# Kernel optimization log

Hardware: AMD Instinct MI355X
Metric: run time of the kernel (lower is better)

The kernel has to match this reference:

```python
import jax, jax.numpy as jnp
import numpy as np


def setup_inputs() -> dict:
    key = jax.random.key(0)
    k1, k2 = jax.random.split(key)
    B, T, H, D = 2, 2048, 16, 64          # batch, seq, heads, head_dim
    NUM_HASHES, NUM_BUCKETS = 4, 64
    hidden_states = jax.random.normal(k1, (B, T, H * D), dtype=jnp.float32)
    # equivalent of torch.randn rotations with fixed hash_seed
    random_rotations = jax.random.normal(k2, (H, D, NUM_HASHES, NUM_BUCKETS // 2), dtype=jnp.float32)
    return {"hidden_states": hidden_states, "random_rotations": random_rotations}


def reference(hidden_states, random_rotations):
    # hidden_states: [B, T, H*D]; random_rotations: [H, D, num_hashes, num_buckets//2]
    H, D, num_hashes, half = random_rotations.shape
    B, T, _ = hidden_states.shape
    # _split_hidden_size_dim: [B,T,H*D] -> [B,H,T,D]
    v = hidden_states.reshape(B, T, H, D).transpose(0, 2, 1, 3)
    # rotated: [B, H, num_hashes, T, num_buckets//2]
    rotated = jnp.einsum('bhtd,hdnr->bhntr', v, random_rotations)
    rotated = jnp.concatenate([rotated, -rotated], axis=-1)  # [..., num_buckets]
    buckets = jnp.argmax(rotated, axis=-1)                   # [B, H, num_hashes, T]
    b = buckets.transpose(0, 1, 3, 2)                        # [B, H, T, num_hashes]
    # m[b,h,i,j] = any_n (bucket_n(i) == bucket_n(j)); OR-accumulate over the
    # small fixed num_hashes axis to avoid a [B,H,T,T,num_hashes] intermediate.
    m = jnp.zeros((B, H, T, T), dtype=bool)
    for n in range(num_hashes):
        bn = b[..., n]
        m = m | (bn[:, :, :, None] == bn[:, :, None, :])
    return m
```

## Files before the change

### kernel.cpp

```cpp
#include <hip/hip_runtime.h>
#include <stdint.h>

#define BB 2
#define HH 16
#define TT 2048
#define DD 64
#define NHASH 4
#define NHALF 32

__global__ __launch_bounds__(256, 3) void lsh_buckets_kernel(
    const float* __restrict__ hs,
    const float* __restrict__ rot,
    uint32_t* __restrict__ words)
{
    __shared__ uint32_t lds[12288];
    float4* v4 = (float4*)lds;
    float4* r4 = (float4*)(lds + 4096);

    const int blk  = blockIdx.x;
    const int bh   = blk >> 5;
    const int tblk = blk & 31;
    const int b    = bh >> 4;
    const int h    = bh & 15;
    const int t0   = tblk * 64;
    const int tid  = threadIdx.x;
    const int n    = tid >> 6;
    const int lane = tid & 63;
    const int tg   = lane >> 3;
    const int rg   = lane & 7;

    #pragma unroll
    for (int p = 0; p < 4; ++p) {
        const int k  = tid + p * 256;
        const int t  = k >> 4;
        const int d4 = k & 15;
        const float4 f = ((const float4*)(hs + ((size_t)(b * TT + t0 + t)) * (HH * DD) + h * DD))[d4];
        v4[t * 16 + (d4 ^ (t >> 3))] = f;
    }
    {
        const float* rh = rot + (size_t)h * (DD * NHASH * NHALF);
        float* rf = (float*)r4;
        #pragma unroll
        for (int p = 0; p < 32; ++p) {
            const int g  = tid + p * 256;
            const int d  = g >> 7;
            const int nr = g & 127;
            const int nn = nr >> 5;
            const int r  = nr & 31;
            const int slot = (d >> 2) ^ (r >> 2);
            rf[((nn * 32 + r) * 16 + slot) * 4 + (d & 3)] = rh[g];
        }
    }
    __syncthreads();

    double acc[8][4];
    #pragma unroll
    for (int i = 0; i < 8; ++i)
        #pragma unroll
        for (int j = 0; j < 4; ++j) acc[i][j] = 0.0;

    const int vbase = tg * 8 * 16;
    const int rbase = (n * 32 + rg * 4) * 16;

    for (int s = 0; s < 16; ++s) {
        double rd[4][4];
        #pragma unroll
        for (int j = 0; j < 4; ++j) {
            const float4 rf = r4[rbase + j * 16 + (s ^ rg)];
            rd[j][0] = (double)rf.x; rd[j][1] = (double)rf.y;
            rd[j][2] = (double)rf.z; rd[j][3] = (double)rf.w;
        }
        #pragma unroll
        for (int i = 0; i < 8; ++i) {
            const float4 vf = v4[vbase + i * 16 + (s ^ tg)];
            const double v0 = (double)vf.x, v1 = (double)vf.y;
            const double v2 = (double)vf.z, v3 = (double)vf.w;
            #pragma unroll
            for (int j = 0; j < 4; ++j) {
                acc[i][j] += v0 * rd[j][0];
                acc[i][j] += v1 * rd[j][1];
                acc[i][j] += v2 * rd[j][2];
                acc[i][j] += v3 * rd[j][3];
            }
        }
    }

    __syncthreads();
    float*    vmaxL = (float*)lds;
    float*    vminL = (float*)(lds + 2304);
    uint32_t* imaxL = lds + 4608;
    uint32_t* iminL = lds + 6912;
    uint32_t* bkt   = lds + 9216;

    #pragma unroll
    for (int i = 0; i < 8; ++i) {
        const int t = tg * 8 + i;
        float fmx = -INFINITY; int imx = 0;
        float fmn =  INFINITY; int imn = 0;
        #pragma unroll
        for (int j = 0; j < 4; ++j) {
            const float f = (float)acc[i][j];
            const int   r = rg * 4 + j;
            if (f > fmx) { fmx = f; imx = r; }
            if (f < fmn) { fmn = f; imn = r; }
        }
        const int o = (n * 64 + t) * 9 + rg;
        vmaxL[o] = fmx; vminL[o] = fmn;
        imaxL[o] = (uint32_t)imx; iminL[o] = (uint32_t)imn;
    }
    __syncthreads();
    {
        const int nn = tid >> 6;
        const int t  = tid & 63;
        float fmx = -INFINITY; int imx = 0;
        float fmn =  INFINITY; int imn = 0;
        #pragma unroll
        for (int g = 0; g < 8; ++g) {
            const int o = (nn * 64 + t) * 9 + g;
            const float fx = vmaxL[o];
            const float fn = vminL[o];
            if (fx > fmx) { fmx = fx; imx = (int)imaxL[o]; }
            if (fn < fmn) { fmn = fn; imn = (int)iminL[o]; }
        }
        const uint32_t bucket = (fmx >= -fmn) ? (uint32_t)imx : (uint32_t)(NHALF + imn);
        bkt[nn * 64 + t] = bucket;
    }
    __syncthreads();
    if (tid < 64) {
        words[(size_t)bh * TT + t0 + tid] = bkt[tid]
                                          | (bkt[64  + tid] << 8)
                                          | (bkt[128 + tid] << 16)
                                          | (bkt[192 + tid] << 24);
    }
}

#define ROWS 32
__device__ __forceinline__ uint32_t eq_any_byte(uint32_t a, uint32_t b) {
    const uint32_t x = a ^ b;
    return ((x - 0x01010101u) & ~x & 0x80808080u) ? 1u : 0u;
}

__global__ __launch_bounds__(512) void lsh_mask_kernel(
    const uint32_t* __restrict__ words,
    uint4* __restrict__ out)
{
    const int bh  = blockIdx.x >> 6;
    const int i0  = (blockIdx.x & 63) * ROWS;
    const int tid = threadIdx.x;
    const uint32_t* wrow = words + (bh << 11);

    const uint4 wj = ((const uint4*)wrow)[tid];

    uint4* op = out + (((size_t)((bh << 11) + i0)) << 9) + tid;
    #pragma unroll
    for (int k = 0; k < ROWS; ++k) {
        const uint32_t wi = wrow[i0 + k];
        uint4 r;
        r.x = eq_any_byte(wi, wj.x); r.y = eq_any_byte(wi, wj.y);
        r.z = eq_any_byte(wi, wj.z); r.w = eq_any_byte(wi, wj.w);
        op[(size_t)k << 9] = r;
    }
}

extern "C" void kernel_launch(void* const* d_in, const int* in_sizes, int n_in,
                              void* d_out, int out_size, void* d_ws, size_t ws_size,
                              hipStream_t stream) {
    const float* hs  = (const float*)d_in[0];
    const float* rot = (const float*)d_in[1];
    uint32_t* words  = (uint32_t*)d_ws;

    lsh_buckets_kernel<<<BB * HH * (TT / 64), 256, 0, stream>>>(hs, rot, words);
    lsh_mask_kernel<<<BB * HH * (TT / ROWS), 512, 0, stream>>>(words, (uint4*)d_out);
}
```

Measured before the change: 126.7 us.

## Process 128 tokens per block and reduce argmax with wave shuffles

The buckets kernel now handles 128 tokens per block in two halves, so each rotation-matrix load into shared memory is reused twice and the grid is halved. The shared-memory argmax reduction with its extra barriers is replaced by xor-shuffle reductions across the 8 lanes, and each bucket byte is written straight to global memory. The trade-offs are lower occupancy (launch bounds drop from 3 to 2 blocks), more shared memory per block, and byte-granular global stores in place of packed 32-bit word stores. The mask kernel, which writes the large output, is unchanged, so the overall effect depends on how much of the total time the buckets kernel takes.

After: 134.3 us. 1.06x slower.

```diff
diff --git a/kernel.cpp b/kernel.cpp
--- a/kernel.cpp
+++ b/kernel.cpp
@@ -8,21 +8,21 @@
 #define NHASH 4
 #define NHALF 32
 
-__global__ __launch_bounds__(256, 3) void lsh_buckets_kernel(
+__global__ __launch_bounds__(256, 2) void lsh_buckets_kernel(
     const float* __restrict__ hs,
     const float* __restrict__ rot,
     uint32_t* __restrict__ words)
 {
-    __shared__ uint32_t lds[12288];
+    __shared__ uint32_t lds[16384];
     float4* v4 = (float4*)lds;
-    float4* r4 = (float4*)(lds + 4096);
+    float4* r4 = (float4*)(lds + 8192);
 
     const int blk  = blockIdx.x;
-    const int bh   = blk >> 5;
-    const int tblk = blk & 31;
+    const int bh   = blk >> 4;
+    const int tblk = blk & 15;
     const int b    = bh >> 4;
     const int h    = bh & 15;
-    const int t0   = tblk * 64;
+    const int t0   = tblk * 128;
     const int tid  = threadIdx.x;
     const int n    = tid >> 6;
     const int lane = tid & 63;
@@ -30,12 +30,12 @@
     const int rg   = lane & 7;
 
     #pragma unroll
-    for (int p = 0; p < 4; ++p) {
+    for (int p = 0; p < 8; ++p) {
         const int k  = tid + p * 256;
         const int t  = k >> 4;
         const int d4 = k & 15;
         const float4 f = ((const float4*)(hs + ((size_t)(b * TT + t0 + t)) * (HH * DD) + h * DD))[d4];
-        v4[t * 16 + (d4 ^ (t >> 3))] = f;
+        v4[t * 16 + (d4 ^ ((t >> 3) & 7))] = f;
     }
     {
         const float* rh = rot + (size_t)h * (DD * NHASH * NHALF);
@@ -53,84 +53,68 @@
     }
     __syncthreads();
 
-    double acc[8][4];
+    const int rbase = (n * 32 + rg * 4) * 16;
+    const int r0    = rg * 4;
+
     #pragma unroll
-    for (int i = 0; i < 8; ++i)
+    for (int half = 0; half < 2; ++half) {
+        const int th0   = half * 64;
+        const int vbase = (th0 + tg * 8) * 16;
+
+        double acc[8][4];
         #pragma unroll
-        for (int j = 0; j < 4; ++j) acc[i][j] = 0.0;
+        for (int i = 0; i < 8; ++i)
+            #pragma unroll
+            for (int j = 0; j < 4; ++j) acc[i][j] = 0.0;
 
-    const int vbase = tg * 8 * 16;
-    const int rbase = (n * 32 + rg * 4) * 16;
+        for (int s = 0; s < 16; ++s) {
+            double rd[4][4];
+            #pragma unroll
+            for (int j = 0; j < 4; ++j) {
+                const float4 rf = r4[rbase + j * 16 + (s ^ rg)];
+                rd[j][0] = (double)rf.x; rd[j][1] = (double)rf.y;
+                rd[j][2] = (double)rf.z; rd[j][3] = (double)rf.w;
+            }
+            #pragma unroll
+            for (int i = 0; i < 8; ++i) {
+                const float4 vf = v4[vbase + i * 16 + (s ^ tg)];
+                const double v0 = (double)vf.x, v1 = (double)vf.y;
+                const double v2 = (double)vf.z, v3 = (double)vf.w;
+                #pragma unroll
+                for (int j = 0; j < 4; ++j) {
+                    acc[i][j] += v0 * rd[j][0];
+                    acc[i][j] += v1 * rd[j][1];
+                    acc[i][j] += v2 * rd[j][2];
+                    acc[i][j] += v3 * rd[j][3];
+                }
+            }
+        }
 
-    for (int s = 0; s < 16; ++s) {
-        double rd[4][4];
-        #pragma unroll
-        for (int j = 0; j < 4; ++j) {
-            const float4 rf = r4[rbase + j * 16 + (s ^ rg)];
-            rd[j][0] = (double)rf.x; rd[j][1] = (double)rf.y;
-            rd[j][2] = (double)rf.z; rd[j][3] = (double)rf.w;
-        }
         #pragma unroll
         for (int i = 0; i < 8; ++i) {
-            const float4 vf = v4[vbase + i * 16 + (s ^ tg)];
-            const double v0 = (double)vf.x, v1 = (double)vf.y;
-            const double v2 = (double)vf.z, v3 = (double)vf.w;
+            float fmx = -INFINITY; int imx = 0;
+            float fmn =  INFINITY; int imn = 0;
             #pragma unroll
             for (int j = 0; j < 4; ++j) {
-                acc[i][j] += v0 * rd[j][0];
-                acc[i][j] += v1 * rd[j][1];
-                acc[i][j] += v2 * rd[j][2];
-                acc[i][j] += v3 * rd[j][3];
+                const float f = (float)acc[i][j];
+                const int   r = r0 + j;
+                if (f > fmx) { fmx = f; imx = r; }
+                if (f < fmn) { fmn = f; imn = r; }
+            }
+            #pragma unroll
+            for (int off = 1; off < 8; off <<= 1) {
+                const float px = __shfl_xor(fmx, off);
+                const int   pi = __shfl_xor(imx, off);
+                const float qx = __shfl_xor(fmn, off);
+                const int   qi = __shfl_xor(imn, off);
+                if (px > fmx || (px == fmx && pi < imx)) { fmx = px; imx = pi; }
+                if (qx < fmn || (qx == fmn && qi < imn)) { fmn = qx; imn = qi; }
+            }
+            if (rg == 0) {
+                const uint32_t bucket = (fmx >= -fmn) ? (uint32_t)imx : (uint32_t)(NHALF + imn);
+                ((uint8_t*)words)[((size_t)bh * TT + t0 + th0 + tg * 8 + i) * 4 + n] = (uint8_t)bucket;
             }
         }
-    }
-
-    __syncthreads();
-    float*    vmaxL = (float*)lds;
-    float*    vminL = (float*)(lds + 2304);
-    uint32_t* imaxL = lds + 4608;
-    uint32_t* iminL = lds + 6912;
-    uint32_t* bkt   = lds + 9216;
-
-    #pragma unroll
-    for (int i = 0; i < 8; ++i) {
-        const int t = tg * 8 + i;
-        float fmx = -INFINITY; int imx = 0;
-        float fmn =  INFINITY; int imn = 0;
-        #pragma unroll
-        for (int j = 0; j < 4; ++j) {
-            const float f = (float)acc[i][j];
-            const int   r = rg * 4 + j;
-            if (f > fmx) { fmx = f; imx = r; }
-            if (f < fmn) { fmn = f; imn = r; }
-        }
-        const int o = (n * 64 + t) * 9 + rg;
-        vmaxL[o] = fmx; vminL[o] = fmn;
-        imaxL[o] = (uint32_t)imx; iminL[o] = (uint32_t)imn;
-    }
-    __syncthreads();
-    {
-        const int nn = tid >> 6;
-        const int t  = tid & 63;
-        float fmx = -INFINITY; int imx = 0;
-        float fmn =  INFINITY; int imn = 0;
-        #pragma unroll
-        for (int g = 0; g < 8; ++g) {
-            const int o = (nn * 64 + t) * 9 + g;
-            const float fx = vmaxL[o];
-            const float fn = vminL[o];
-            if (fx > fmx) { fmx = fx; imx = (int)imaxL[o]; }
-            if (fn < fmn) { fmn = fn; imn = (int)iminL[o]; }
-        }
-        const uint32_t bucket = (fmx >= -fmn) ? (uint32_t)imx : (uint32_t)(NHALF + imn);
-        bkt[nn * 64 + t] = bucket;
-    }
-    __syncthreads();
-    if (tid < 64) {
-        words[(size_t)bh * TT + t0 + tid] = bkt[tid]
-                                          | (bkt[64  + tid] << 8)
-                                          | (bkt[128 + tid] << 16)
-                                          | (bkt[192 + tid] << 24);
     }
 }
 
@@ -169,6 +153,6 @@
     const float* rot = (const float*)d_in[1];
     uint32_t* words  = (uint32_t*)d_ws;
 
-    lsh_buckets_kernel<<<BB * HH * (TT / 64), 256, 0, stream>>>(hs, rot, words);
+    lsh_buckets_kernel<<<BB * HH * (TT / 128), 256, 0, stream>>>(hs, rot, words);
     lsh_mask_kernel<<<BB * HH * (TT / ROWS), 512, 0, stream>>>(words, (uint4*)d_out);
 }
```

## Compute LSH projections in fp32 with fp64 recompute for ambiguous argmax

Applied to the files above, without the earlier changes.

Switches the rotation GEMM accumulation from fp64 to fp32. Any token whose top-two max/min margins fall below a small certainty threshold is flagged in an LDS bitmask and recomputed exactly in fp64 by a wavefront. The cross-lane argmax reduction now uses wave shuffles instead of LDS staging, which removes one barrier phase. The approach assumes the fp32 error stays below the threshold, and ambiguous tokens add serial per-wave work.

After: 130.2 us. 1.03x slower.

```diff
diff --git a/kernel.cpp b/kernel.cpp
--- a/kernel.cpp
+++ b/kernel.cpp
@@ -7,13 +7,14 @@
 #define DD 64
 #define NHASH 4
 #define NHALF 32
+#define GCERT 0.00390625f
 
 __global__ __launch_bounds__(256, 3) void lsh_buckets_kernel(
     const float* __restrict__ hs,
     const float* __restrict__ rot,
     uint32_t* __restrict__ words)
 {
-    __shared__ uint32_t lds[12288];
+    __shared__ uint32_t lds[12552];
     float4* v4 = (float4*)lds;
     float4* r4 = (float4*)(lds + 4096);
 
@@ -29,6 +30,8 @@
     const int tg   = lane >> 3;
     const int rg   = lane & 7;
 
+    if (tid < 8) lds[12544 + tid] = 0;
+
     #pragma unroll
     for (int p = 0; p < 4; ++p) {
         const int k  = tid + p * 256;
@@ -53,84 +56,112 @@
     }
     __syncthreads();
 
-    double acc[8][4];
+    float acc[8][4];
     #pragma unroll
     for (int i = 0; i < 8; ++i)
         #pragma unroll
-        for (int j = 0; j < 4; ++j) acc[i][j] = 0.0;
+        for (int j = 0; j < 4; ++j) acc[i][j] = 0.0f;
 
     const int vbase = tg * 8 * 16;
     const int rbase = (n * 32 + rg * 4) * 16;
+    const int r0    = rg * 4;
 
     for (int s = 0; s < 16; ++s) {
-        double rd[4][4];
-        #pragma unroll
-        for (int j = 0; j < 4; ++j) {
-            const float4 rf = r4[rbase + j * 16 + (s ^ rg)];
-            rd[j][0] = (double)rf.x; rd[j][1] = (double)rf.y;
-            rd[j][2] = (double)rf.z; rd[j][3] = (double)rf.w;
-        }
+        float4 rd[4];
+        #pragma unroll
+        for (int j = 0; j < 4; ++j) rd[j] = r4[rbase + j * 16 + (s ^ rg)];
         #pragma unroll
         for (int i = 0; i < 8; ++i) {
             const float4 vf = v4[vbase + i * 16 + (s ^ tg)];
-            const double v0 = (double)vf.x, v1 = (double)vf.y;
-            const double v2 = (double)vf.z, v3 = (double)vf.w;
             #pragma unroll
             for (int j = 0; j < 4; ++j) {
-                acc[i][j] += v0 * rd[j][0];
-                acc[i][j] += v1 * rd[j][1];
-                acc[i][j] += v2 * rd[j][2];
-                acc[i][j] += v3 * rd[j][3];
+                acc[i][j] += vf.x * rd[j].x;
+                acc[i][j] += vf.y * rd[j].y;
+                acc[i][j] += vf.z * rd[j].z;
+                acc[i][j] += vf.w * rd[j].w;
             }
         }
     }
 
+    #pragma unroll
+    for (int i = 0; i < 8; ++i) {
+        float m1 = -INFINITY, m2 = -INFINITY; int i1 = 0;
+        float n1 =  INFINITY, n2 =  INFINITY; int j1 = 0;
+        #pragma unroll
+        for (int j = 0; j < 4; ++j) {
+            const float f = acc[i][j];
+            const int   r = r0 + j;
+            if (f > m1) { m2 = m1; m1 = f; i1 = r; } else if (f > m2) m2 = f;
+            if (f < n1) { n2 = n1; n1 = f; j1 = r; } else if (f < n2) n2 = f;
+        }
+        #pragma unroll
+        for (int off = 1; off < 8; off <<= 1) {
+            const float pm1 = __shfl_xor(m1, off); const int pi1 = __shfl_xor(i1, off);
+            const float pm2 = __shfl_xor(m2, off);
+            const float pn1 = __shfl_xor(n1, off); const int pj1 = __shfl_xor(j1, off);
+            const float pn2 = __shfl_xor(n2, off);
+            if (pm1 > m1 || (pm1 == m1 && pi1 < i1)) { m2 = fmaxf(m1, pm2); m1 = pm1; i1 = pi1; }
+            else                                     { m2 = fmaxf(m2, pm1); }
+            if (pn1 < n1 || (pn1 == n1 && pj1 < j1)) { n2 = fminf(n1, pn2); n1 = pn1; j1 = pj1; }
+            else                                     { n2 = fminf(n2, pn1); }
+        }
+        if (rg == 0) {
+            const int t = tg * 8 + i;
+            const bool cert = (m1 - m2 > GCERT) && (n2 - n1 > GCERT) && (fabsf(m1 + n1) > GCERT);
+            lds[12288 + n * 64 + t] = (m1 >= -n1) ? (uint32_t)i1 : (uint32_t)(NHALF + j1);
+            if (!cert)
+                atomicOr(&lds[12544 + n * 2 + (t >> 5)], 1u << (t & 31));
+        }
+    }
     __syncthreads();
-    float*    vmaxL = (float*)lds;
-    float*    vminL = (float*)(lds + 2304);
-    uint32_t* imaxL = lds + 4608;
-    uint32_t* iminL = lds + 6912;
-    uint32_t* bkt   = lds + 9216;
-
-    #pragma unroll
-    for (int i = 0; i < 8; ++i) {
-        const int t = tg * 8 + i;
-        float fmx = -INFINITY; int imx = 0;
-        float fmn =  INFINITY; int imn = 0;
-        #pragma unroll
-        for (int j = 0; j < 4; ++j) {
-            const float f = (float)acc[i][j];
-            const int   r = rg * 4 + j;
-            if (f > fmx) { fmx = f; imx = r; }
-            if (f < fmn) { fmn = f; imn = r; }
-        }
-        const int o = (n * 64 + t) * 9 + rg;
-        vmaxL[o] = fmx; vminL[o] = fmn;
-        imaxL[o] = (uint32_t)imx; iminL[o] = (uint32_t)imn;
+
+    {
+        uint32_t mlo = lds[12544 + n * 2];
+        uint32_t mhi = lds[12544 + n * 2 + 1];
+        const int r    = lane & 31;
+        const int hsel = lane >> 5;
+        const int rb2  = (n * 32 + r) * 16;
+        const int rsw  = r >> 2;
+        while (mlo | mhi) {
+            int t;
+            if (mlo) { t = __ffs(mlo) - 1;      mlo &= mlo - 1; }
+            else     { t = 32 + __ffs(mhi) - 1; mhi &= mhi - 1; }
+            double a0 = 0.0, a1 = 0.0;
+            const int tb  = t * 16;
+            const int tsw = t >> 3;
+            #pragma unroll
+            for (int c = 0; c < 8; ++c) {
+                const int d4 = hsel * 8 + c;
+                const float4 vf = v4[tb + (d4 ^ tsw)];
+                const float4 rf = r4[rb2 + (d4 ^ rsw)];
+                a0 += (double)vf.x * (double)rf.x;
+                a1 += (double)vf.y * (double)rf.y;
+                a0 += (double)vf.z * (double)rf.z;
+                a1 += (double)vf.w * (double)rf.w;
+            }
+            double dsum = a0 + a1;
+            dsum += __shfl_xor(dsum, 32);
+            const float f = (float)dsum;
+            float fmx = f; int imx = r;
+            float fmn = f; int imn = r;
+            #pragma unroll
+            for (int off = 1; off < 32; off <<= 1) {
+                const float px = __shfl_xor(fmx, off, 32); const int pix = __shfl_xor(imx, off, 32);
+                const float qn = __shfl_xor(fmn, off, 32); const int qin = __shfl_xor(imn, off, 32);
+                if (px > fmx || (px == fmx && pix < imx)) { fmx = px; imx = pix; }
+                if (qn < fmn || (qn == fmn && qin < imn)) { fmn = qn; imn = qin; }
+            }
+            if (lane == 0)
+                lds[12288 + n * 64 + t] = (fmx >= -fmn) ? (uint32_t)imx : (uint32_t)(NHALF + imn);
+        }
     }
     __syncthreads();
-    {
-        const int nn = tid >> 6;
-        const int t  = tid & 63;
-        float fmx = -INFINITY; int imx = 0;
-        float fmn =  INFINITY; int imn = 0;
-        #pragma unroll
-        for (int g = 0; g < 8; ++g) {
-            const int o = (nn * 64 + t) * 9 + g;
-            const float fx = vmaxL[o];
-            const float fn = vminL[o];
-            if (fx > fmx) { fmx = fx; imx = (int)imaxL[o]; }
-            if (fn < fmn) { fmn = fn; imn = (int)iminL[o]; }
-        }
-        const uint32_t bucket = (fmx >= -fmn) ? (uint32_t)imx : (uint32_t)(NHALF + imn);
-        bkt[nn * 64 + t] = bucket;
-    }
-    __syncthreads();
+
     if (tid < 64) {
-        words[(size_t)bh * TT + t0 + tid] = bkt[tid]
-                                          | (bkt[64  + tid] << 8)
-                                          | (bkt[128 + tid] << 16)
-                                          | (bkt[192 + tid] << 24);
+        words[(size_t)bh * TT + t0 + tid] = lds[12288 + tid]
+                                          | (lds[12288 + 64  + tid] << 8)
+                                          | (lds[12288 + 128 + tid] << 16)
+                                          | (lds[12288 + 192 + tid] << 24);
     }
 }
 
```
